# Optimization experiments

Hardware: AMD Instinct MI355X
Metric: run time of the kernel (lower is better)

## Reference

```python
import jax, jax.numpy as jnp
import numpy as np

B, D, T_STEPS = 256, 512, 256


def setup_inputs() -> dict:
    key = jax.random.key(0)
    k1, k2 = jax.random.split(key)
    # Scale K like flax lecun_normal init (std = 1/sqrt(fan_in)) so rollout stays stable.
    z0 = jax.random.normal(k1, (B, D), dtype=jnp.float32)
    K = jax.random.normal(k2, (D, D), dtype=jnp.float32) / np.sqrt(D)
    return {"z0": z0, "K": K, "T": T_STEPS}


def reference(z0, K, T):
    # z_{t+1} = z_t @ K  (flax Linear with use_bias=False: y = x @ kernel)
    def step(z, _):
        z_next = z @ K  # [B, D] @ [D, D] -> [B, D]
        return z_next, z_next

    _, preds = jax.lax.scan(step, z0, xs=None, length=T)  # [T, B, D]
    return jnp.transpose(preds, (1, 0, 2))  # [B, T, D]
```

## Files before the change

### kernel.cpp

```cpp
#include <hip/hip_runtime.h>


typedef unsigned short u16;
typedef unsigned int u32;
typedef __bf16 bf16x8 __attribute__((ext_vector_type(8)));
typedef float f32x4 __attribute__((ext_vector_type(4)));
typedef u16 u16x4 __attribute__((ext_vector_type(4)));
typedef u16 u16x8 __attribute__((ext_vector_type(8)));

#define MAT 262144
#define SLOT 1048576
#define WSLOT 131072

__device__ __forceinline__ u16 f2b(float f) {
  u32 x = __float_as_uint(f);
  return (u16)((x + 0x7fffu + ((x >> 16) & 1u)) >> 16);
}
__device__ __forceinline__ float b2f(u16 u) { return __uint_as_float(((u32)u) << 16); }

__device__ __forceinline__ size_t pidx(int r, int k) {
  return (size_t)(((r >> 4) * 16 + (k >> 5)) * 512 + ((k >> 3) & 3) * 128 + (r & 15) * 8 + (k & 7));
}

__device__ __forceinline__ void gll16(const void* g, void* l) {
  __builtin_amdgcn_global_load_lds((__attribute__((address_space(1))) void*)(void*)g,
                                   (__attribute__((address_space(3))) void*)l, 16, 0, 0);
}

__global__ __launch_bounds__(256) void prep_kernel(const float* __restrict__ Kc,
                                                   const float* __restrict__ z0,
                                                   u16* __restrict__ P,
                                                   u16* __restrict__ W0,
                                                   u16* __restrict__ z0lo) {
  int tid = threadIdx.x, b = blockIdx.x;
  if (b < 64) {
    int r0 = (b >> 3) * 64, c0b = (b & 7) * 64;
#pragma unroll
    for (int q = 0; q < 2; ++q) {
      int g = q * 256 + tid;
      int r = r0 + (g >> 3), c0 = c0b + (g & 7) * 8;
      float4 v0 = *(const float4*)(Kc + (size_t)r * 512 + c0);
      float4 v1 = *(const float4*)(Kc + (size_t)r * 512 + c0 + 4);
      float v[8] = {v0.x, v0.y, v0.z, v0.w, v1.x, v1.y, v1.z, v1.w};
      u16x8 h8, l8v;
#pragma unroll
      for (int j = 0; j < 8; ++j) {
        u16 h = f2b(v[j]);
        h8[j] = h;
        l8v[j] = f2b(v[j] - b2f(h));
        size_t ib = pidx(c0 + j, r);
        P[2 * MAT + ib] = h;
        P[3 * MAT + ib] = l8v[j];
      }
      size_t ia = pidx(r, c0);
      *(u16x8*)(P + ia) = h8;
      *(u16x8*)(P + MAT + ia) = l8v;
    }
  } else {
    int idb = b - 64;
#pragma unroll
    for (int q = 0; q < 4; ++q) {
      int g = (idb * 4 + q) * 256 + tid;
      int r = g >> 6, c0 = (g & 63) * 8;
      float4 v0 = *(const float4*)(z0 + (size_t)r * 512 + c0);
      float4 v1 = *(const float4*)(z0 + (size_t)r * 512 + c0 + 4);
      float v[8] = {v0.x, v0.y, v0.z, v0.w, v1.x, v1.y, v1.z, v1.w};
      u16x8 h8, l8v;
#pragma unroll
      for (int j = 0; j < 8; ++j) {
        u16 h = f2b(v[j]);
        h8[j] = h;
        l8v[j] = f2b(v[j] - b2f(h));
      }
      size_t ia = pidx(r, c0);
      *(u16x8*)(W0 + ia) = h8;
      *(u16x8*)(z0lo + ia) = l8v;
    }
  }
}

__global__ __launch_bounds__(256, 2) void gemm_split(
    const u16* __restrict__ A0h, const u16* __restrict__ A0l, long Astr,
    const u16* __restrict__ B0h, long Bstr,
    u16* __restrict__ C0, long Cstr, int wmode) {
  __shared__ u16 Bs[32768];
  int z = blockIdx.z;
  const u16* Ah = A0h + (size_t)z * Astr;
  const u16* Al = A0l + (size_t)z * Astr;
  const u16* Bh = B0h + (size_t)z * Bstr;
  const u16* Bl = Bh + MAT;
  u16* C = C0 + (size_t)z * Cstr;
  int tid = threadIdx.x;
  int m0 = blockIdx.y * 64, n0 = blockIdx.x * 32;
  int wv = tid >> 6, lane = tid & 63;
  int mrow = lane & 15, quad = lane >> 4;
  int l8 = lane * 8;
  int nchunk0 = n0 >> 4;
  const u16* ph = Bh + (size_t)nchunk0 * 16 * 512;
  const u16* pl = Bl + (size_t)nchunk0 * 16 * 512;
#pragma unroll
  for (int i = 0; i < 8; ++i) {
    int ch = wv * 8 + i;
    gll16(ph + (size_t)ch * 512 + l8, Bs + ch * 512);
    gll16(pl + (size_t)ch * 512 + l8, Bs + 16384 + ch * 512);
  }
  __syncthreads();
  int mc = (m0 >> 4) + wv;
  f32x4 acc[2] = {};
#pragma unroll 4
  for (int kt = 0; kt < 16; ++kt) {
    size_t co = (size_t)(mc * 16 + kt) * 512 + l8;
    bf16x8 ah = *(const bf16x8*)(Ah + co);
    bf16x8 al = *(const bf16x8*)(Al + co);
#pragma unroll
    for (int nt = 0; nt < 2; ++nt) {
      bf16x8 bh = *(const bf16x8*)(Bs + (nt * 16 + kt) * 512 + l8);
      bf16x8 bl = *(const bf16x8*)(Bs + 16384 + (nt * 16 + kt) * 512 + l8);
      acc[nt] = __builtin_amdgcn_mfma_f32_16x16x32_bf16(ah, bh, acc[nt], 0, 0, 0);
      acc[nt] = __builtin_amdgcn_mfma_f32_16x16x32_bf16(al, bh, acc[nt], 0, 0, 0);
      acc[nt] = __builtin_amdgcn_mfma_f32_16x16x32_bf16(ah, bl, acc[nt], 0, 0, 0);
    }
  }
  int mbase = m0 + wv * 16 + quad * 4;
#pragma unroll
  for (int nt = 0; nt < 2; ++nt) {
    int n = n0 + nt * 16 + mrow;
    if (wmode == 0) {
      u16x4 h4, l4;
#pragma unroll
      for (int r = 0; r < 4; ++r) {
        float v = acc[nt][r];
        u16 h = f2b(v), l = f2b(v - b2f(h));
        size_t ia = pidx(mbase + r, n);
        C[ia] = h;
        C[MAT + ia] = l;
        h4[r] = h;
        l4[r] = l;
      }
      size_t ib = pidx(n, mbase);
      *(u16x4*)(C + 2 * MAT + ib) = h4;
      *(u16x4*)(C + 3 * MAT + ib) = l4;
    } else {
#pragma unroll
      for (int r = 0; r < 4; ++r) C[pidx(mbase + r, n)] = f2b(acc[nt][r]);
    }
  }
}

__global__ __launch_bounds__(256, 2) void gemm_out(const u16* __restrict__ Wb,
                                                   const u16* __restrict__ PT0,
                                                   float* __restrict__ out) {
  __shared__ u16 Bs[32768];
  int z = blockIdx.z;
  const u16* A = Wb + (size_t)(z >> 4) * WSLOT;
  const u16* Bt = PT0 + (size_t)(z & 15) * SLOT;
  int tid = threadIdx.x;
  int n0 = blockIdx.x * 64;
  int wv = tid >> 6, lane = tid & 63;
  int mrow = lane & 15, quad = lane >> 4;
  int l8 = lane * 8;
  const u16* pb = Bt + (size_t)(n0 >> 4) * 16 * 512;
#pragma unroll
  for (int i = 0; i < 16; ++i) {
    int ch = wv * 16 + i;
    gll16(pb + (size_t)ch * 512 + l8, Bs + ch * 512);
  }
  __syncthreads();
  int mc0 = wv * 4;
  f32x4 acc[4][4] = {};
#pragma unroll 4
  for (int kt = 0; kt < 16; ++kt) {
    bf16x8 a[4], b[4];
#pragma unroll
    for (int mt = 0; mt < 4; ++mt)
      a[mt] = *(const bf16x8*)(A + (size_t)((mc0 + mt) * 16 + kt) * 512 + l8);
#pragma unroll
    for (int nt = 0; nt < 4; ++nt)
      b[nt] = *(const bf16x8*)(Bs + (nt * 16 + kt) * 512 + l8);
#pragma unroll
    for (int mt = 0; mt < 4; ++mt)
#pragma unroll
      for (int nt = 0; nt < 4; ++nt)
        acc[mt][nt] = __builtin_amdgcn_mfma_f32_16x16x32_bf16(a[mt], b[nt], acc[mt][nt], 0, 0, 0);
  }
#pragma unroll
  for (int mt = 0; mt < 4; ++mt)
#pragma unroll
    for (int nt = 0; nt < 4; ++nt) {
      int gb = wv * 64 + mt * 16 + quad * 4;
      int gd = n0 + nt * 16 + mrow;
#pragma unroll
      for (int r = 0; r < 4; ++r)
        out[((size_t)(gb + r) * 256 + z) * 512 + gd] = acc[mt][nt][r];
    }
}

extern "C" void kernel_launch(void* const* d_in, const int* in_sizes, int n_in,
                              void* d_out, int out_size, void* d_ws, size_t ws_size,
                              hipStream_t stream) {
  const float* z0 = (const float*)d_in[0];
  const float* Kc = (const float*)d_in[1];
  float* out = (float*)d_out;
  u16* W = (u16*)d_ws;
  u16* z0l = W + 16 * WSLOT;
  u16* P = z0l + WSLOT;
  auto S = [&](int s) { return P + (size_t)s * SLOT; };
  dim3 blk(256);

  prep_kernel<<<80, blk, 0, stream>>>(Kc, z0, P, W, z0l);
  gemm_split<<<dim3(16, 8, 1), blk, 0, stream>>>(S(0), S(0) + MAT, 0, S(0) + 2 * MAT, 0, S(1), 0, 0);
  gemm_split<<<dim3(16, 8, 2), blk, 0, stream>>>(S(0), S(0) + MAT, SLOT, S(1) + 2 * MAT, 0, S(2), SLOT, 0);
  gemm_split<<<dim3(16, 8, 4), blk, 0, stream>>>(S(0), S(0) + MAT, SLOT, S(3) + 2 * MAT, 0, S(4), SLOT, 0);
  gemm_split<<<dim3(16, 8, 8), blk, 0, stream>>>(S(0), S(0) + MAT, SLOT, S(7) + 2 * MAT, 0, S(8), SLOT, 0);
  gemm_split<<<dim3(16, 8, 1), blk, 0, stream>>>(S(15), S(15) + MAT, 0, S(15) + 2 * MAT, 0, S(16), 0, 0);
  gemm_split<<<dim3(16, 8, 2), blk, 0, stream>>>(S(16), S(16) + MAT, 0, S(15) + 2 * MAT, SLOT, S(17), SLOT, 0);
  gemm_split<<<dim3(16, 8, 4), blk, 0, stream>>>(S(18), S(18) + MAT, 0, S(15) + 2 * MAT, SLOT, S(19), SLOT, 0);
  gemm_split<<<dim3(16, 8, 7), blk, 0, stream>>>(S(22), S(22) + MAT, 0, S(15) + 2 * MAT, SLOT, S(23), SLOT, 0);
  gemm_split<<<dim3(16, 4, 15), blk, 0, stream>>>(W, z0l, 0, S(15) + 2 * MAT, SLOT, W + WSLOT, WSLOT, 1);
  gemm_out<<<dim3(8, 1, 256), blk, 0, stream>>>(W, P + 2 * MAT, out);
}
```

Before: 261.9 us.

## Fuse matrix-power ladder launches into one persistent kernel with grid barriers

The nine dependent gemm_split launches that build powers of K and the W basis are replaced by a single persistent 256-workgroup kernel. It walks the nine levels with a software grid barrier between them and reuses the LDS-staged B tile when consecutive tasks share it. gemm_out is reindexed into a flat grid with a swizzled tile order, meant to improve L2 locality. The goal is to remove per-launch overhead and tail idle time between small dependent GEMMs, at the cost of spin-barrier overhead and a deadlock risk if not all 256 workgroups are co-resident.

Measured after the change: 670.6 us. 2.56x slower.

```diff
diff --git a/kernel.cpp b/kernel.cpp
--- a/kernel.cpp
+++ b/kernel.cpp
@@ -11,6 +11,7 @@
 #define MAT 262144
 #define SLOT 1048576
 #define WSLOT 131072
+#define P0 (17 * WSLOT)
 
 __device__ __forceinline__ u16 f2b(float f) {
   u32 x = __float_as_uint(f);
@@ -27,12 +28,32 @@
                                    (__attribute__((address_space(3))) void*)l, 16, 0, 0);
 }
 
+__device__ __forceinline__ void grid_barrier(u32* bar) {
+  __syncthreads();
+  if (threadIdx.x == 0) {
+    __threadfence();
+    u32* cnt = bar;
+    u32* gen = bar + 32;
+    u32 g = __hip_atomic_load(gen, __ATOMIC_RELAXED, __HIP_MEMORY_SCOPE_AGENT);
+    u32 a = __hip_atomic_fetch_add(cnt, 1u, __ATOMIC_ACQ_REL, __HIP_MEMORY_SCOPE_AGENT);
+    if (a == gridDim.x - 1) {
+      __hip_atomic_store(cnt, 0u, __ATOMIC_RELAXED, __HIP_MEMORY_SCOPE_AGENT);
+      __hip_atomic_store(gen, g + 1u, __ATOMIC_RELEASE, __HIP_MEMORY_SCOPE_AGENT);
+    } else {
+      while (__hip_atomic_load(gen, __ATOMIC_ACQUIRE, __HIP_MEMORY_SCOPE_AGENT) == g)
+        __builtin_amdgcn_s_sleep(8);
+    }
+    __threadfence();
+  }
+  __syncthreads();
+}
+
 __global__ __launch_bounds__(256) void prep_kernel(const float* __restrict__ Kc,
                                                    const float* __restrict__ z0,
-                                                   u16* __restrict__ P,
-                                                   u16* __restrict__ W0,
-                                                   u16* __restrict__ z0lo) {
+                                                   u16* __restrict__ ws, u32* __restrict__ bar) {
   int tid = threadIdx.x, b = blockIdx.x;
+  u16* P = ws + P0;
+  if (b == 0 && tid == 0) { bar[0] = 0; bar[32] = 0; }
   if (b < 64) {
     int r0 = (b >> 3) * 64, c0b = (b & 7) * 64;
 #pragma unroll
@@ -58,6 +79,8 @@
     }
   } else {
     int idb = b - 64;
+    u16* W0 = ws;
+    u16* z0lo = ws + 16 * WSLOT;
 #pragma unroll
     for (int q = 0; q < 4; ++q) {
       int g = (idb * 4 + q) * 256 + tid;
@@ -79,71 +102,97 @@
   }
 }
 
-__global__ __launch_bounds__(256, 2) void gemm_split(
-    const u16* __restrict__ A0h, const u16* __restrict__ A0l, long Astr,
-    const u16* __restrict__ B0h, long Bstr,
-    u16* __restrict__ C0, long Cstr, int wmode) {
+#define SL(s) (P0 + (s) * SLOT)
+__global__ __launch_bounds__(256, 2) void ladder_kernel(u16* __restrict__ ws, u32* __restrict__ bar) {
   __shared__ u16 Bs[32768];
-  int z = blockIdx.z;
-  const u16* Ah = A0h + (size_t)z * Astr;
-  const u16* Al = A0l + (size_t)z * Astr;
-  const u16* Bh = B0h + (size_t)z * Bstr;
-  const u16* Bl = Bh + MAT;
-  u16* C = C0 + (size_t)z * Cstr;
-  int tid = threadIdx.x;
-  int m0 = blockIdx.y * 64, n0 = blockIdx.x * 32;
+  const int AH[9] = {SL(0), SL(0), SL(0), SL(0), SL(15), SL(15), SL(15), SL(15), 0};
+  const int AL[9] = {SL(0) + MAT, SL(0) + MAT, SL(0) + MAT, SL(0) + MAT,
+                     SL(15) + MAT, SL(15) + MAT, SL(15) + MAT, SL(15) + MAT, 16 * WSLOT};
+  const int ASTR[9] = {0, SLOT, SLOT, SLOT, 0, SLOT, SLOT, SLOT, 0};
+  const int BH[9] = {SL(0) + 2 * MAT, SL(1) + 2 * MAT, SL(3) + 2 * MAT, SL(7) + 2 * MAT,
+                     SL(15) + 2 * MAT, SL(16) + 2 * MAT, SL(18) + 2 * MAT, SL(22) + 2 * MAT,
+                     SL(15) + 2 * MAT};
+  const int BSTR[9] = {0, 0, 0, 0, 0, 0, 0, 0, SLOT};
+  const int CO[9] = {SL(1), SL(2), SL(4), SL(8), SL(16), SL(17), SL(19), SL(23), WSLOT};
+  const int CSTR[9] = {0, SLOT, SLOT, SLOT, 0, SLOT, SLOT, SLOT, WSLOT};
+  const int ZC[9] = {1, 2, 4, 8, 1, 2, 4, 7, 15};
+  const int MTC[9] = {8, 8, 8, 8, 8, 8, 8, 8, 4};
+  int wg = blockIdx.x, tid = threadIdx.x;
+  int vw = ((wg & 7) << 5) | (wg >> 3);
   int wv = tid >> 6, lane = tid & 63;
-  int mrow = lane & 15, quad = lane >> 4;
-  int l8 = lane * 8;
-  int nchunk0 = n0 >> 4;
-  const u16* ph = Bh + (size_t)nchunk0 * 16 * 512;
-  const u16* pl = Bl + (size_t)nchunk0 * 16 * 512;
-#pragma unroll
-  for (int i = 0; i < 8; ++i) {
-    int ch = wv * 8 + i;
-    gll16(ph + (size_t)ch * 512 + l8, Bs + ch * 512);
-    gll16(pl + (size_t)ch * 512 + l8, Bs + 16384 + ch * 512);
-  }
-  __syncthreads();
-  int mc = (m0 >> 4) + wv;
-  f32x4 acc[2] = {};
+  int mrow = lane & 15, quad = lane >> 4, l8 = lane * 8;
+  long prevKey = -1;
+  for (int L = 0; L < 9; ++L) {
+    int z = ZC[L], mt = MTC[L], wm = (L == 8);
+    int T = z * mt * 16;
+    int per = (T + 255) >> 8;
+    int t0 = vw * per, t1 = t0 + per;
+    if (t1 > T) t1 = T;
+    for (int t = t0; t < t1; ++t) {
+      int n = t / (z * mt);
+      int rem = t - n * (z * mt);
+      int zi = rem / mt, m = rem - zi * mt;
+      const u16* Bh = ws + BH[L] + (long)zi * BSTR[L];
+      const u16* ph = Bh + (long)n * 16384;
+      long key = (long)(ph - ws) + ((long)L << 40);
+      if (key != prevKey) {
+        __syncthreads();
+        const u16* pl = ph + MAT;
+#pragma unroll
+        for (int i = 0; i < 8; ++i) {
+          int ch = wv * 8 + i;
+          gll16(ph + (long)ch * 512 + l8, Bs + ch * 512);
+          gll16(pl + (long)ch * 512 + l8, Bs + 16384 + ch * 512);
+        }
+        __syncthreads();
+        prevKey = key;
+      }
+      const u16* Ah = ws + AH[L] + (long)zi * ASTR[L];
+      const u16* Al = ws + AL[L] + (long)zi * ASTR[L];
+      u16* C = ws + CO[L] + (long)zi * CSTR[L];
+      int m0 = m * 64, n0 = n * 32;
+      int mc = (m0 >> 4) + wv;
+      f32x4 acc[2] = {};
 #pragma unroll 4
-  for (int kt = 0; kt < 16; ++kt) {
-    size_t co = (size_t)(mc * 16 + kt) * 512 + l8;
-    bf16x8 ah = *(const bf16x8*)(Ah + co);
-    bf16x8 al = *(const bf16x8*)(Al + co);
-#pragma unroll
-    for (int nt = 0; nt < 2; ++nt) {
-      bf16x8 bh = *(const bf16x8*)(Bs + (nt * 16 + kt) * 512 + l8);
-      bf16x8 bl = *(const bf16x8*)(Bs + 16384 + (nt * 16 + kt) * 512 + l8);
-      acc[nt] = __builtin_amdgcn_mfma_f32_16x16x32_bf16(ah, bh, acc[nt], 0, 0, 0);
-      acc[nt] = __builtin_amdgcn_mfma_f32_16x16x32_bf16(al, bh, acc[nt], 0, 0, 0);
-      acc[nt] = __builtin_amdgcn_mfma_f32_16x16x32_bf16(ah, bl, acc[nt], 0, 0, 0);
-    }
-  }
-  int mbase = m0 + wv * 16 + quad * 4;
-#pragma unroll
-  for (int nt = 0; nt < 2; ++nt) {
-    int n = n0 + nt * 16 + mrow;
-    if (wmode == 0) {
-      u16x4 h4, l4;
-#pragma unroll
-      for (int r = 0; r < 4; ++r) {
-        float v = acc[nt][r];
-        u16 h = f2b(v), l = f2b(v - b2f(h));
-        size_t ia = pidx(mbase + r, n);
-        C[ia] = h;
-        C[MAT + ia] = l;
-        h4[r] = h;
-        l4[r] = l;
-      }
-      size_t ib = pidx(n, mbase);
-      *(u16x4*)(C + 2 * MAT + ib) = h4;
-      *(u16x4*)(C + 3 * MAT + ib) = l4;
-    } else {
-#pragma unroll
-      for (int r = 0; r < 4; ++r) C[pidx(mbase + r, n)] = f2b(acc[nt][r]);
-    }
+      for (int kt = 0; kt < 16; ++kt) {
+        long co = (long)(mc * 16 + kt) * 512 + l8;
+        bf16x8 ah = *(const bf16x8*)(Ah + co);
+        bf16x8 al = *(const bf16x8*)(Al + co);
+#pragma unroll
+        for (int nt = 0; nt < 2; ++nt) {
+          bf16x8 bh = *(const bf16x8*)(Bs + (nt * 16 + kt) * 512 + l8);
+          bf16x8 bl = *(const bf16x8*)(Bs + 16384 + (nt * 16 + kt) * 512 + l8);
+          acc[nt] = __builtin_amdgcn_mfma_f32_16x16x32_bf16(ah, bh, acc[nt], 0, 0, 0);
+          acc[nt] = __builtin_amdgcn_mfma_f32_16x16x32_bf16(al, bh, acc[nt], 0, 0, 0);
+          acc[nt] = __builtin_amdgcn_mfma_f32_16x16x32_bf16(ah, bl, acc[nt], 0, 0, 0);
+        }
+      }
+      int mbase = m0 + wv * 16 + quad * 4;
+#pragma unroll
+      for (int nt = 0; nt < 2; ++nt) {
+        int nn = n0 + nt * 16 + mrow;
+        if (!wm) {
+          u16x4 h4, l4;
+#pragma unroll
+          for (int r = 0; r < 4; ++r) {
+            float v = acc[nt][r];
+            u16 h = f2b(v), l = f2b(v - b2f(h));
+            size_t ia = pidx(mbase + r, nn);
+            C[ia] = h;
+            C[MAT + ia] = l;
+            h4[r] = h;
+            l4[r] = l;
+          }
+          size_t ib = pidx(nn, mbase);
+          *(u16x4*)(C + 2 * MAT + ib) = h4;
+          *(u16x4*)(C + 3 * MAT + ib) = l4;
+        } else {
+#pragma unroll
+          for (int r = 0; r < 4; ++r) C[pidx(mbase + r, nn)] = f2b(acc[nt][r]);
+        }
+      }
+    }
+    if (L < 8) grid_barrier(bar);
   }
 }
 
@@ -151,18 +200,20 @@
                                                    const u16* __restrict__ PT0,
                                                    float* __restrict__ out) {
   __shared__ u16 Bs[32768];
-  int z = blockIdx.z;
-  const u16* A = Wb + (size_t)(z >> 4) * WSLOT;
-  const u16* Bt = PT0 + (size_t)(z & 15) * SLOT;
+  int zz = blockIdx.x;
+  int i = (zz & 3) | (((zz >> 3) & 3) << 2);
+  int j = ((zz >> 2) & 1) | (((zz >> 5) & 7) << 1);
+  int n0 = (zz >> 8) * 64;
+  int t = j * 16 + i;
+  const u16* A = Wb + (size_t)j * WSLOT;
+  const u16* Bt = PT0 + (size_t)i * SLOT;
   int tid = threadIdx.x;
-  int n0 = blockIdx.x * 64;
   int wv = tid >> 6, lane = tid & 63;
-  int mrow = lane & 15, quad = lane >> 4;
-  int l8 = lane * 8;
+  int mrow = lane & 15, quad = lane >> 4, l8 = lane * 8;
   const u16* pb = Bt + (size_t)(n0 >> 4) * 16 * 512;
 #pragma unroll
-  for (int i = 0; i < 16; ++i) {
-    int ch = wv * 16 + i;
+  for (int q = 0; q < 16; ++q) {
+    int ch = wv * 16 + q;
     gll16(pb + (size_t)ch * 512 + l8, Bs + ch * 512);
   }
   __syncthreads();
@@ -191,7 +242,7 @@
       int gd = n0 + nt * 16 + mrow;
 #pragma unroll
       for (int r = 0; r < 4; ++r)
-        out[((size_t)(gb + r) * 256 + z) * 512 + gd] = acc[mt][nt][r];
+        out[((size_t)(gb + r) * 256 + t) * 512 + gd] = acc[mt][nt][r];
     }
 }
 
@@ -201,21 +252,10 @@
   const float* z0 = (const float*)d_in[0];
   const float* Kc = (const float*)d_in[1];
   float* out = (float*)d_out;
-  u16* W = (u16*)d_ws;
-  u16* z0l = W + 16 * WSLOT;
-  u16* P = z0l + WSLOT;
-  auto S = [&](int s) { return P + (size_t)s * SLOT; };
+  u16* ws = (u16*)d_ws;
+  u32* bar = (u32*)(ws + (size_t)P0 + 30 * (size_t)SLOT);
   dim3 blk(256);
-
-  prep_kernel<<<80, blk, 0, stream>>>(Kc, z0, P, W, z0l);
-  gemm_split<<<dim3(16, 8, 1), blk, 0, stream>>>(S(0), S(0) + MAT, 0, S(0) + 2 * MAT, 0, S(1), 0, 0);
-  gemm_split<<<dim3(16, 8, 2), blk, 0, stream>>>(S(0), S(0) + MAT, SLOT, S(1) + 2 * MAT, 0, S(2), SLOT, 0);
-  gemm_split<<<dim3(16, 8, 4), blk, 0, stream>>>(S(0), S(0) + MAT, SLOT, S(3) + 2 * MAT, 0, S(4), SLOT, 0);
-  gemm_split<<<dim3(16, 8, 8), blk, 0, stream>>>(S(0), S(0) + MAT, SLOT, S(7) + 2 * MAT, 0, S(8), SLOT, 0);
-  gemm_split<<<dim3(16, 8, 1), blk, 0, stream>>>(S(15), S(15) + MAT, 0, S(15) + 2 * MAT, 0, S(16), 0, 0);
-  gemm_split<<<dim3(16, 8, 2), blk, 0, stream>>>(S(16), S(16) + MAT, 0, S(15) + 2 * MAT, SLOT, S(17), SLOT, 0);
-  gemm_split<<<dim3(16, 8, 4), blk, 0, stream>>>(S(18), S(18) + MAT, 0, S(15) + 2 * MAT, SLOT, S(19), SLOT, 0);
-  gemm_split<<<dim3(16, 8, 7), blk, 0, stream>>>(S(22), S(22) + MAT, 0, S(15) + 2 * MAT, SLOT, S(23), SLOT, 0);
-  gemm_split<<<dim3(16, 4, 15), blk, 0, stream>>>(W, z0l, 0, S(15) + 2 * MAT, SLOT, W + WSLOT, WSLOT, 1);
-  gemm_out<<<dim3(8, 1, 256), blk, 0, stream>>>(W, P + 2 * MAT, out);
-}
+  prep_kernel<<<80, blk, 0, stream>>>(Kc, z0, ws, bar);
+  ladder_kernel<<<256, blk, 0, stream>>>(ws, bar);
+  gemm_out<<<2048, blk, 0, stream>>>(ws, ws + P0 + 2 * MAT, out);
+}
```
